# Kernel optimization log

Measured on AMD Instinct MI355X. Metric: run time of the kernel, lower is better.

The kernel has to match this reference:

```python
import math
import jax, jax.numpy as jnp
import numpy as np


def positional_encoding(c, h, w):
    # Faithful port of the torch positional_encode grid (c divisible by 4).
    half = c // 2
    div = jnp.exp(jnp.arange(0, half, 2, dtype=jnp.float32) * (-math.log(10000.0) / half))  # [half/2]
    pos_w = jnp.arange(w, dtype=jnp.float32)[:, None]  # [w,1]
    pos_h = jnp.arange(h, dtype=jnp.float32)[:, None]  # [h,1]
    q = half // 2
    pe = jnp.zeros((c, h, w), dtype=jnp.float32)
    sw = jnp.sin(pos_w * div).T[:, None, :]  # [q,1,w] -> broadcast over height
    cw = jnp.cos(pos_w * div).T[:, None, :]
    sh = jnp.sin(pos_h * div).T[:, :, None]  # [q,h,1] -> broadcast over width
    ch = jnp.cos(pos_h * div).T[:, :, None]
    pe = pe.at[0:half:2].set(jnp.broadcast_to(sw, (q, h, w)))
    pe = pe.at[1:half:2].set(jnp.broadcast_to(cw, (q, h, w)))
    pe = pe.at[half::2].set(jnp.broadcast_to(sh, (q, h, w)))
    pe = pe.at[half + 1::2].set(jnp.broadcast_to(ch, (q, h, w)))
    return pe


def setup_inputs() -> dict:
    key = jax.random.key(0)
    k1, k2, k3, k4 = jax.random.split(key, 4)
    b, c, h, w = 4, 256, 64, 64
    x = jax.random.normal(k1, (b, c, h, w), dtype=jnp.float32)
    # kaiming_uniform-ish scale for d x d weights
    bound = 1.0 / math.sqrt(c)
    Wq = jax.random.uniform(k2, (c, c), dtype=jnp.float32, minval=-bound, maxval=bound)
    Wk = jax.random.uniform(k3, (c, c), dtype=jnp.float32, minval=-bound, maxval=bound)
    Wv = jax.random.uniform(k4, (c, c), dtype=jnp.float32, minval=-bound, maxval=bound)
    return {"x": x, "Wq": Wq, "Wk": Wk, "Wv": Wv}


def reference(x, Wq, Wk, Wv):
    b, c, h, w = x.shape
    pe = positional_encoding(c, h, w)
    xt = (x + pe).reshape(b, c, h * w).transpose(0, 2, 1)  # [b, hw, c]
    Q = xt @ Wq  # [b, hw, c]
    K = xt @ Wk
    V = xt @ Wv
    scores = jnp.einsum('bqc,bkc->bqk', Q, K) / math.sqrt(c)  # [b, hw, hw]
    # NOTE: softmax over dim=1 (the QUERY axis), matching nn.Softmax(dim=1)
    A = jax.nn.softmax(scores, axis=1)
    out = jnp.einsum('bqk,bkc->bqc', A, V)  # [b, hw, c]
    return out.transpose(0, 2, 1).reshape(b, c, h, w)
```

## Files before the change

### kernel.cpp

```cpp
#include <hip/hip_runtime.h>
#include <hip/hip_bf16.h>
#include <math.h>

typedef float f32x4 __attribute__((ext_vector_type(4)));
typedef short bf16x8 __attribute__((ext_vector_type(8)));
typedef short bf16x4 __attribute__((ext_vector_type(4)));

#define AS1 __attribute__((address_space(1)))
#define AS3 __attribute__((address_space(3)))

__device__ __forceinline__ short f2bf(float f) {
    unsigned u = __float_as_uint(f);
    unsigned r = (u + 0x7fffu + ((u >> 16) & 1u)) >> 16;
    return (short)r;
}
__device__ __forceinline__ float bf2f(short s) {
    return __uint_as_float(((unsigned)(unsigned short)s) << 16);
}
__device__ __forceinline__ void gld16(const void* g, void* l) {
    __builtin_amdgcn_global_load_lds((const AS1 unsigned int*)g, (AS3 unsigned int*)l, 16, 0, 0);
}

__device__ __forceinline__ void stage128x64(const short* __restrict__ g,
                                            short* lds, int t) {
    int w = t >> 6, l = t & 63;
    #pragma unroll
    for (int j = 0; j < 4; ++j) {
        int ii = j * 4 + w;
        int row = ii * 8 + (l >> 3);
        int slot = (l & 7) ^ (row & 7);
        gld16(g + row * 256 + slot * 8, lds + ii * 512);
    }
}

__device__ __forceinline__ void stage64x64(const short* __restrict__ g,
                                           short* lds, int t) {
    #pragma unroll
    for (int j = 0; j < 2; ++j) {
        int idx = j * 256 + t;
        int row = idx >> 3;
        int slot = (idx & 7) ^ (row & 7);
        gld16(g + (size_t)row * 4096 + slot * 8, lds + idx * 8);
    }
}

__device__ __forceinline__ void stage128x64v(const short* __restrict__ g,
                                             short* lds, int t) {
    #pragma unroll
    for (int j = 0; j < 4; ++j) {
        int idx = j * 256 + t;
        int row = idx >> 3;
        int slot = (idx & 7) ^ (row & 7);
        gld16(g + (size_t)row * 4096 + slot * 8, lds + idx * 8);
    }
}

__global__ __launch_bounds__(256) void k_prep(const float* __restrict__ x,
                                              const float* __restrict__ Wq,
                                              const float* __restrict__ Wk,
                                              const float* __restrict__ Wv,
                                              short* __restrict__ xt,
                                              short* __restrict__ Wt) {
    int bidx = blockIdx.x;
    if (bidx < 768) {
        int wsel = bidx >> 8, n = bidx & 255, k = threadIdx.x;
        const float* W = (wsel == 0) ? Wq : (wsel == 1) ? Wk : Wv;
        Wt[(wsel * 256 + n) * 256 + k] = f2bf(W[k * 256 + n]);
        return;
    }
    int bid = bidx - 768;
    int b = bid >> 7;
    int pb = bid & 127;
    __shared__ __align__(16) float tile[256][33];
    __shared__ __align__(16) float pew[128][32];
    __shared__ __align__(16) float peh[128];
    int t = threadIdx.x;
    const float c1 = 0.14391156f;
    int wbase = (pb & 1) * 32;
    int hpos = pb >> 1;
    #pragma unroll
    for (int j = 0; j < 16; ++j) {
        int idx = t + j * 256;
        int c = idx >> 5, pp = idx & 31;
        int i = c >> 1;
        float d = expf(-(float)i * c1);
        float arg = (float)(wbase + pp) * d;
        pew[c][pp] = (c & 1) ? cosf(arg) : sinf(arg);
    }
    if (t < 128) {
        int i = t >> 1;
        float d = expf(-(float)i * c1);
        float arg = (float)hpos * d;
        peh[t] = (t & 1) ? cosf(arg) : sinf(arg);
    }
    int p0 = pb * 32;
    #pragma unroll
    for (int j = 0; j < 32; ++j) {
        int c = j * 8 + (t >> 5);
        int pp = t & 31;
        tile[c][pp] = x[((b * 256 + c) << 12) + p0 + pp];
    }
    __syncthreads();
    int pp = t >> 3, cseg = t & 7;
    int p = p0 + pp;
    short* dst = xt + (((b << 12) + p) << 8) + (cseg << 5);
    #pragma unroll
    for (int j = 0; j < 4; ++j) {
        bf16x8 v;
        #pragma unroll
        for (int e = 0; e < 8; ++e) {
            int c = cseg * 32 + j * 8 + e;
            float pe = (c < 128) ? pew[c][pp] : peh[c - 128];
            v[e] = f2bf(tile[c][pp] + pe);
        }
        ((bf16x8*)dst)[j] = v;
    }
}

__global__ __launch_bounds__(256, 4) void k_proj(const short* __restrict__ xt,
                                                 const short* __restrict__ Wt,
                                                 short* __restrict__ Q,
                                                 short* __restrict__ K,
                                                 short* __restrict__ VT) {
    int id = blockIdx.x;
    int wsel = id % 3; id /= 3;
    int nt = id & 1;  id >>= 1;
    int mt = id & 31; int b = id >> 5;
    int t = threadIdx.x, l = t & 63, w = t >> 6;
    int lr = l & 15, lg = l >> 4;
    int wr = w >> 1, wc = w & 1;
    __shared__ __align__(16) short Xa[128 * 64];
    __shared__ __align__(16) short Wa[128 * 64];
    const short* Xg = xt + (((size_t)b << 12) + mt * 128) * 256;
    const short* Wg = Wt + ((size_t)wsel * 256 + nt * 128) * 256;
    f32x4 acc[4][4] = {};

    #pragma unroll
    for (int ks = 0; ks < 4; ++ks) {
        stage128x64(Xg + ks * 64, Xa, t);
        stage128x64(Wg + ks * 64, Wa, t);
        __syncthreads();
        #pragma unroll
        for (int s = 0; s < 2; ++s) {
            bf16x8 af[4], bw[4];
            #pragma unroll
            for (int ms = 0; ms < 4; ++ms) {
                int row = wr * 64 + ms * 16 + lr;
                af[ms] = *(const bf16x8*)(Xa + row * 64 + (((s * 4 + lg) ^ (row & 7)) << 3));
            }
            #pragma unroll
            for (int fn = 0; fn < 4; ++fn) {
                int row = wc * 64 + fn * 16 + lr;
                bw[fn] = *(const bf16x8*)(Wa + row * 64 + (((s * 4 + lg) ^ (row & 7)) << 3));
            }
            #pragma unroll
            for (int ms = 0; ms < 4; ++ms)
                #pragma unroll
                for (int fn = 0; fn < 4; ++fn)
                    acc[ms][fn] = __builtin_amdgcn_mfma_f32_16x16x32_bf16(af[ms], bw[fn], acc[ms][fn], 0, 0, 0);
        }
        __syncthreads();
    }

    int m0 = mt * 128 + wr * 64;
    int n0 = nt * 128 + wc * 64;
    if (wsel < 2) {
        float scl = (wsel == 0) ? 0.0625f : 1.0f;
        short* dst = (wsel == 0) ? Q : K;
        #pragma unroll
        for (int ms = 0; ms < 4; ++ms)
            #pragma unroll
            for (int fn = 0; fn < 4; ++fn)
                #pragma unroll
                for (int r = 0; r < 4; ++r) {
                    int m = m0 + ms * 16 + lg * 4 + r;
                    int n = n0 + fn * 16 + lr;
                    dst[((b << 12) + m) * 256 + n] = f2bf(acc[ms][fn][r] * scl);
                }
    } else {
        #pragma unroll
        for (int ms = 0; ms < 4; ++ms)
            #pragma unroll
            for (int fn = 0; fn < 4; ++fn) {
                int n = n0 + fn * 16 + lr;
                int m = m0 + ms * 16 + lg * 4;
                bf16x4 v;
                #pragma unroll
                for (int r = 0; r < 4; ++r) v[r] = f2bf(acc[ms][fn][r]);
                *(bf16x4*)(VT + ((b * 256 + n) << 12) + m) = v;
            }
    }
}

__global__ __launch_bounds__(256, 4) void k_E(const short* __restrict__ Qm,
                                              const short* __restrict__ Km,
                                              short* __restrict__ E,
                                              float* __restrict__ pl) {
    int o = blockIdx.x;
    int bid = (o & 7) * 512 + (o >> 3);
    int qt = bid & 31, kt = (bid >> 5) & 31, b = bid >> 10;
    int t = threadIdx.x, l = t & 63;
    int w = t >> 6;
    int wr = w >> 1, wc = w & 1;
    int lr = l & 15, lg = l >> 4;
    __shared__ __align__(16) short Ka[128 * 64];
    __shared__ __align__(16) short Qa[128 * 64];
    __shared__ float plds[128];
    const short* Kg = Km + (((size_t)b << 12) + kt * 128) * 256;
    const short* Qg = Qm + (((size_t)b << 12) + qt * 128) * 256;
    f32x4 acc[4][4] = {};

    #pragma unroll
    for (int ks = 0; ks < 4; ++ks) {
        stage128x64(Kg + ks * 64, Ka, t);
        stage128x64(Qg + ks * 64, Qa, t);
        __syncthreads();
        #pragma unroll
        for (int s = 0; s < 2; ++s) {
            bf16x8 a[4], bq[4];
            #pragma unroll
            for (int mk = 0; mk < 4; ++mk) {
                int row = wr * 64 + mk * 16 + lr;
                a[mk] = *(const bf16x8*)(Ka + row * 64 + (((s * 4 + lg) ^ (row & 7)) << 3));
            }
            #pragma unroll
            for (int nq = 0; nq < 4; ++nq) {
                int row = wc * 64 + nq * 16 + lr;
                bq[nq] = *(const bf16x8*)(Qa + row * 64 + (((s * 4 + lg) ^ (row & 7)) << 3));
            }
            #pragma unroll
            for (int mk = 0; mk < 4; ++mk)
                #pragma unroll
                for (int nq = 0; nq < 4; ++nq)
                    acc[mk][nq] = __builtin_amdgcn_mfma_f32_16x16x32_bf16(a[mk], bq[nq], acc[mk][nq], 0, 0, 0);
        }
        __syncthreads();
    }

    int k0 = kt * 128 + wr * 64;
    int q0 = qt * 128 + wc * 64;
    float psum[4][4];
    #pragma unroll
    for (int mk = 0; mk < 4; ++mk) {
        float ps0 = 0.f, ps1 = 0.f, ps2 = 0.f, ps3 = 0.f;
        #pragma unroll
        for (int nq = 0; nq < 4; ++nq) {
            int q = q0 + nq * 16 + lr;
            float e0 = __expf(acc[mk][nq][0]);
            float e1 = __expf(acc[mk][nq][1]);
            float e2 = __expf(acc[mk][nq][2]);
            float e3 = __expf(acc[mk][nq][3]);
            ps0 += e0; ps1 += e1; ps2 += e2; ps3 += e3;
            bf16x4 ev;
            ev[0] = f2bf(e0); ev[1] = f2bf(e1); ev[2] = f2bf(e2); ev[3] = f2bf(e3);
            *(bf16x4*)(E + (((size_t)b << 12) + q) * 4096 + k0 + mk * 16 + lg * 4) = ev;
        }
        psum[mk][0] = ps0; psum[mk][1] = ps1; psum[mk][2] = ps2; psum[mk][3] = ps3;
    }
    #pragma unroll
    for (int mk = 0; mk < 4; ++mk)
        #pragma unroll
        for (int r = 0; r < 4; ++r) {
            float v = psum[mk][r];
            v += __shfl_xor(v, 1);
            v += __shfl_xor(v, 2);
            v += __shfl_xor(v, 4);
            v += __shfl_xor(v, 8);
            psum[mk][r] = v;
        }
    if (wc == 0 && lr == 0) {
        #pragma unroll
        for (int mk = 0; mk < 4; ++mk)
            #pragma unroll
            for (int r = 0; r < 4; ++r)
                plds[wr * 64 + mk * 16 + lg * 4 + r] = psum[mk][r];
    }
    __syncthreads();
    if (wc == 1 && lr == 0) {
        #pragma unroll
        for (int mk = 0; mk < 4; ++mk)
            #pragma unroll
            for (int r = 0; r < 4; ++r)
                plds[wr * 64 + mk * 16 + lg * 4 + r] += psum[mk][r];
    }
    __syncthreads();
    if (t < 128) pl[(b * 32 + qt) * 4096 + kt * 128 + t] = plds[t];
}

__global__ void k_lred(const float* __restrict__ pl, float* __restrict__ rl) {
    int gid = blockIdx.x * 256 + threadIdx.x;
    float s = 0.f;
    int b = gid >> 12, k = gid & 4095;
    #pragma unroll
    for (int qt = 0; qt < 32; ++qt) s += pl[(b * 32 + qt) * 4096 + k];
    rl[gid] = 1.0f / s;
}

__global__ void k_vn(const short* __restrict__ VT, const float* __restrict__ rl,
                     short* __restrict__ Vnt) {
    int gid = blockIdx.x * 256 + threadIdx.x;
    int idx8 = gid * 8;
    int b = idx8 >> 20;
    int rem = idx8 & 1048575;
    int k = rem & 4095;
    bf16x8 v = *(const bf16x8*)(VT + idx8);
    const float* rb = rl + (b << 12) + k;
    f32x4 r0 = *(const f32x4*)(rb);
    f32x4 r1 = *(const f32x4*)(rb + 4);
    bf16x8 oo;
    #pragma unroll
    for (int e = 0; e < 8; ++e) {
        float f = bf2f(v[e]);
        float rr = (e < 4) ? r0[e] : r1[e - 4];
        oo[e] = f2bf(f * rr);
    }
    *(bf16x8*)(Vnt + idx8) = oo;
}

__global__ __launch_bounds__(256) void k_pv(const short* __restrict__ E,
                                            const short* __restrict__ Vnt,
                                            float* __restrict__ out) {
    int o = blockIdx.x;
    int ct = o >> 8;
    int r = o & 255;
    int b = r >> 6, qt = r & 63;
    int t = threadIdx.x, l = t & 63, w = t >> 6;
    int wq = w >> 1, wc = w & 1;
    int lr = l & 15, lg = l >> 4;
    int q0 = qt * 64, c0 = ct * 128;
    __shared__ __align__(16) short Ea[64 * 64];
    __shared__ __align__(16) short Va[128 * 64];
    const short* Eg = E + (((size_t)b << 12) + q0) * 4096;
    const short* Vg = Vnt + ((size_t)(b * 256 + c0)) * 4096;
    f32x4 acc[2][4] = {};

    for (int kc = 0; kc < 4096; kc += 64) {
        stage64x64(Eg + kc, Ea, t);
        stage128x64v(Vg + kc, Va, t);
        __syncthreads();
        bf16x8 Af[2][2], Bf[4][2];
        #pragma unroll
        for (int s = 0; s < 2; ++s) {
            #pragma unroll
            for (int mq = 0; mq < 2; ++mq) {
                int row = wq * 32 + mq * 16 + lr;
                Af[mq][s] = *(const bf16x8*)(Ea + row * 64 + (((s * 4 + lg) ^ (row & 7)) << 3));
            }
            #pragma unroll
            for (int nc = 0; nc < 4; ++nc) {
                int row = wc * 64 + nc * 16 + lr;
                Bf[nc][s] = *(const bf16x8*)(Va + row * 64 + (((s * 4 + lg) ^ (row & 7)) << 3));
            }
        }
        #pragma unroll
        for (int s = 0; s < 2; ++s)
            #pragma unroll
            for (int mq = 0; mq < 2; ++mq)
                #pragma unroll
                for (int nc = 0; nc < 4; ++nc)
                    acc[mq][nc] = __builtin_amdgcn_mfma_f32_16x16x32_bf16(Af[mq][s], Bf[nc][s], acc[mq][nc], 0, 0, 0);
        __syncthreads();
    }
    #pragma unroll
    for (int mq = 0; mq < 2; ++mq)
        #pragma unroll
        for (int nc = 0; nc < 4; ++nc) {
            int c = c0 + wc * 64 + nc * 16 + lr;
            int q = q0 + wq * 32 + mq * 16 + lg * 4;
            *(f32x4*)(out + (((size_t)b << 8) + c) * 4096 + q) = acc[mq][nc];
        }
}

extern "C" void kernel_launch(void* const* d_in, const int* in_sizes, int n_in,
                              void* d_out, int out_size, void* d_ws, size_t ws_size,
                              hipStream_t stream) {
    const float* x  = (const float*)d_in[0];
    const float* Wq = (const float*)d_in[1];
    const float* Wk = (const float*)d_in[2];
    const float* Wv = (const float*)d_in[3];

    char* p = (char*)d_ws;
    short* xt  = (short*)p; p += 4 * 4096 * 256 * 2;
    short* Wt  = (short*)p; p += 3 * 256 * 256 * 2;
    short* Qm  = (short*)p; p += 4 * 4096 * 256 * 2;
    short* Km  = (short*)p; p += 4 * 4096 * 256 * 2;
    short* VT  = (short*)p; p += 4 * 4096 * 256 * 2;
    short* E   = (short*)p; p += (size_t)4 * 4096 * 4096 * 2;
    float* pl  = (float*)p; p += 4 * 32 * 4096 * 4;
    float* rl  = (float*)p; p += 4 * 4096 * 4;
    short* Vnt = (short*)p; p += 4 * 4096 * 256 * 2;

    float* out = (float*)d_out;

    k_prep <<<1280, 256, 0, stream>>>(x, Wq, Wk, Wv, xt, Wt);
    k_proj <<<768, 256, 0, stream>>>(xt, Wt, Qm, Km, VT);
    k_E    <<<4096, 256, 0, stream>>>(Qm, Km, E, pl);
    k_lred <<<64,   256, 0, stream>>>(pl, rl);
    k_vn   <<<2048, 256, 0, stream>>>(VT, rl, Vnt);
    k_pv   <<<512,  256, 0, stream>>>(E, Vnt, out);
}
```

Before: 164.7 us.

## Widen PV blocks to cover all channels and remap blocks per XCD

The PV kernel now uses 512-thread blocks that compute all 256 output channels for a 64-query tile, so each E tile is loaded from memory once instead of twice. Block indices are permuted so neighbouring blocks of the same batch run on the same XCD, improving L2 reuse of V. The cost is a larger LDS footprint and only one block per CU, which lowers occupancy and latency hiding.

```diff
diff --git a/kernel.cpp b/kernel.cpp
--- a/kernel.cpp
+++ b/kernel.cpp
@@ -30,28 +30,6 @@
         int row = ii * 8 + (l >> 3);
         int slot = (l & 7) ^ (row & 7);
         gld16(g + row * 256 + slot * 8, lds + ii * 512);
-    }
-}
-
-__device__ __forceinline__ void stage64x64(const short* __restrict__ g,
-                                           short* lds, int t) {
-    #pragma unroll
-    for (int j = 0; j < 2; ++j) {
-        int idx = j * 256 + t;
-        int row = idx >> 3;
-        int slot = (idx & 7) ^ (row & 7);
-        gld16(g + (size_t)row * 4096 + slot * 8, lds + idx * 8);
-    }
-}
-
-__device__ __forceinline__ void stage128x64v(const short* __restrict__ g,
-                                             short* lds, int t) {
-    #pragma unroll
-    for (int j = 0; j < 4; ++j) {
-        int idx = j * 256 + t;
-        int row = idx >> 3;
-        int slot = (idx & 7) ^ (row & 7);
-        gld16(g + (size_t)row * 4096 + slot * 8, lds + idx * 8);
     }
 }
 
@@ -317,26 +295,34 @@
     *(bf16x8*)(Vnt + idx8) = oo;
 }
 
-__global__ __launch_bounds__(256) void k_pv(const short* __restrict__ E,
+__global__ __launch_bounds__(512) void k_pv(const short* __restrict__ E,
                                             const short* __restrict__ Vnt,
                                             float* __restrict__ out) {
     int o = blockIdx.x;
-    int ct = o >> 8;
-    int r = o & 255;
-    int b = r >> 6, qt = r & 63;
+    int bid = (o & 7) * 32 + (o >> 3);
+    int b = bid >> 6, qt = bid & 63;
     int t = threadIdx.x, l = t & 63, w = t >> 6;
-    int wq = w >> 1, wc = w & 1;
+    int wq = w >> 2, wc = w & 3;
     int lr = l & 15, lg = l >> 4;
-    int q0 = qt * 64, c0 = ct * 128;
+    int q0 = qt * 64;
     __shared__ __align__(16) short Ea[64 * 64];
-    __shared__ __align__(16) short Va[128 * 64];
+    __shared__ __align__(16) short Va[256 * 64];
     const short* Eg = E + (((size_t)b << 12) + q0) * 4096;
-    const short* Vg = Vnt + ((size_t)(b * 256 + c0)) * 4096;
+    const short* Vg = Vnt + ((size_t)b << 20);
     f32x4 acc[2][4] = {};
 
+    int erow = t >> 3, eslot = (t & 7) ^ ((t >> 3) & 7);
     for (int kc = 0; kc < 4096; kc += 64) {
-        stage64x64(Eg + kc, Ea, t);
-        stage128x64v(Vg + kc, Va, t);
+        if (t < 512) {
+            gld16(Eg + kc + (size_t)erow * 4096 + eslot * 8, Ea + t * 8);
+        }
+        #pragma unroll
+        for (int j = 0; j < 4; ++j) {
+            int idx = j * 512 + t;
+            int row = idx >> 3;
+            int slot = (idx & 7) ^ (row & 7);
+            gld16(Vg + kc + (size_t)row * 4096 + slot * 8, Va + idx * 8);
+        }
         __syncthreads();
         bf16x8 Af[2][2], Bf[4][2];
         #pragma unroll
@@ -365,7 +351,7 @@
     for (int mq = 0; mq < 2; ++mq)
         #pragma unroll
         for (int nc = 0; nc < 4; ++nc) {
-            int c = c0 + wc * 64 + nc * 16 + lr;
+            int c = wc * 64 + nc * 16 + lr;
             int q = q0 + wq * 32 + mq * 16 + lg * 4;
             *(f32x4*)(out + (((size_t)b << 8) + c) * 4096 + q) = acc[mq][nc];
         }
@@ -397,5 +383,5 @@
     k_E    <<<4096, 256, 0, stream>>>(Qm, Km, E, pl);
     k_lred <<<64,   256, 0, stream>>>(pl, rl);
     k_vn   <<<2048, 256, 0, stream>>>(VT, rl, Vnt);
-    k_pv   <<<512,  256, 0, stream>>>(E, Vnt, out);
-}
+    k_pv   <<<256,  512, 0, stream>>>(E, Vnt, out);
+}
```

Measured after the change: 176.6 us. 1.07x slower.

## Enlarge k_E tile to 128x256 with 512-thread blocks sharing K tile

Applied to the files above, without the earlier changes.

The score/exp kernel now uses 512-thread blocks covering 256 queries by 128 keys, so each staged K tile is reused by twice as many query rows and fewer blocks are launched. Partial column sums are combined across four warp groups in LDS with a single barrier instead of two, and the row-sum reduction loops over 16 query tiles instead of 32. This lowers redundant K loads and per-block overhead, at the cost of more LDS per block (48KB) and possibly lower occupancy.

```diff
diff --git a/kernel.cpp b/kernel.cpp
--- a/kernel.cpp
+++ b/kernel.cpp
@@ -192,40 +192,52 @@
     }
 }
 
-__global__ __launch_bounds__(256, 4) void k_E(const short* __restrict__ Qm,
-                                              const short* __restrict__ Km,
-                                              short* __restrict__ E,
-                                              float* __restrict__ pl) {
+__global__ __launch_bounds__(512) void k_E(const short* __restrict__ Qm,
+                                           const short* __restrict__ Km,
+                                           short* __restrict__ E,
+                                           float* __restrict__ pl) {
     int o = blockIdx.x;
-    int bid = (o & 7) * 512 + (o >> 3);
-    int qt = bid & 31, kt = (bid >> 5) & 31, b = bid >> 10;
+    int bid = (o & 7) * 256 + (o >> 3);
+    int qt = bid & 15, kt = (bid >> 4) & 31, b = bid >> 9;
     int t = threadIdx.x, l = t & 63;
     int w = t >> 6;
-    int wr = w >> 1, wc = w & 1;
+    int wrk = w & 1, wcq = w >> 1;
     int lr = l & 15, lg = l >> 4;
     __shared__ __align__(16) short Ka[128 * 64];
-    __shared__ __align__(16) short Qa[128 * 64];
-    __shared__ float plds[128];
+    __shared__ __align__(16) short Qa[256 * 64];
+    __shared__ float plds[4 * 128];
     const short* Kg = Km + (((size_t)b << 12) + kt * 128) * 256;
-    const short* Qg = Qm + (((size_t)b << 12) + qt * 128) * 256;
+    const short* Qg = Qm + (((size_t)b << 12) + qt * 256) * 256;
     f32x4 acc[4][4] = {};
 
     #pragma unroll
     for (int ks = 0; ks < 4; ++ks) {
-        stage128x64(Kg + ks * 64, Ka, t);
-        stage128x64(Qg + ks * 64, Qa, t);
+        #pragma unroll
+        for (int j = 0; j < 2; ++j) {
+            int idx = j * 512 + t;
+            int row = idx >> 3;
+            int slot = (idx & 7) ^ (row & 7);
+            gld16(Kg + ks * 64 + row * 256 + slot * 8, Ka + idx * 8);
+        }
+        #pragma unroll
+        for (int j = 0; j < 4; ++j) {
+            int idx = j * 512 + t;
+            int row = idx >> 3;
+            int slot = (idx & 7) ^ (row & 7);
+            gld16(Qg + ks * 64 + row * 256 + slot * 8, Qa + idx * 8);
+        }
         __syncthreads();
         #pragma unroll
         for (int s = 0; s < 2; ++s) {
             bf16x8 a[4], bq[4];
             #pragma unroll
             for (int mk = 0; mk < 4; ++mk) {
-                int row = wr * 64 + mk * 16 + lr;
+                int row = wrk * 64 + mk * 16 + lr;
                 a[mk] = *(const bf16x8*)(Ka + row * 64 + (((s * 4 + lg) ^ (row & 7)) << 3));
             }
             #pragma unroll
             for (int nq = 0; nq < 4; ++nq) {
-                int row = wc * 64 + nq * 16 + lr;
+                int row = wcq * 64 + nq * 16 + lr;
                 bq[nq] = *(const bf16x8*)(Qa + row * 64 + (((s * 4 + lg) ^ (row & 7)) << 3));
             }
             #pragma unroll
@@ -237,8 +249,8 @@
         __syncthreads();
     }
 
-    int k0 = kt * 128 + wr * 64;
-    int q0 = qt * 128 + wc * 64;
+    int k0 = kt * 128 + wrk * 64;
+    int q0 = qt * 256 + wcq * 64;
     float psum[4][4];
     #pragma unroll
     for (int mk = 0; mk < 4; ++mk) {
@@ -268,23 +280,18 @@
             v += __shfl_xor(v, 8);
             psum[mk][r] = v;
         }
-    if (wc == 0 && lr == 0) {
+    if (lr == 0) {
         #pragma unroll
         for (int mk = 0; mk < 4; ++mk)
             #pragma unroll
             for (int r = 0; r < 4; ++r)
-                plds[wr * 64 + mk * 16 + lg * 4 + r] = psum[mk][r];
+                plds[wcq * 128 + wrk * 64 + mk * 16 + lg * 4 + r] = psum[mk][r];
     }
     __syncthreads();
-    if (wc == 1 && lr == 0) {
-        #pragma unroll
-        for (int mk = 0; mk < 4; ++mk)
-            #pragma unroll
-            for (int r = 0; r < 4; ++r)
-                plds[wr * 64 + mk * 16 + lg * 4 + r] += psum[mk][r];
-    }
-    __syncthreads();
-    if (t < 128) pl[(b * 32 + qt) * 4096 + kt * 128 + t] = plds[t];
+    if (t < 128) {
+        float s = plds[t] + plds[128 + t] + plds[256 + t] + plds[384 + t];
+        pl[(b * 16 + qt) * 4096 + kt * 128 + t] = s;
+    }
 }
 
 __global__ void k_lred(const float* __restrict__ pl, float* __restrict__ rl) {
@@ -292,7 +299,7 @@
     float s = 0.f;
     int b = gid >> 12, k = gid & 4095;
     #pragma unroll
-    for (int qt = 0; qt < 32; ++qt) s += pl[(b * 32 + qt) * 4096 + k];
+    for (int qt = 0; qt < 16; ++qt) s += pl[(b * 16 + qt) * 4096 + k];
     rl[gid] = 1.0f / s;
 }
 
@@ -394,7 +401,7 @@
 
     k_prep <<<1280, 256, 0, stream>>>(x, Wq, Wk, Wv, xt, Wt);
     k_proj <<<768, 256, 0, stream>>>(xt, Wt, Qm, Km, VT);
-    k_E    <<<4096, 256, 0, stream>>>(Qm, Km, E, pl);
+    k_E    <<<2048, 512, 0, stream>>>(Qm, Km, E, pl);
     k_lred <<<64,   256, 0, stream>>>(pl, rl);
     k_vn   <<<2048, 256, 0, stream>>>(VT, rl, Vnt);
     k_pv   <<<512,  256, 0, stream>>>(E, Vnt, out);
```

Result: faster. 159.6 us (-3.1%).
